# Optimization experiments

Hardware: AMD Instinct MI355X
Metric: run time of the kernel (lower is better)

The kernel has to match this reference:

```python
import jax, jax.numpy as jnp
import numpy as np

H, W = 256, 256
N_PIXELS = H * W
MAX_DIST = float(np.sqrt(H ** 2 + W ** 2))
RESIZED = jnp.array([H, W], dtype=jnp.float32)

# all_img_locations: cartesian product of rows x cols, shape [N_PIXELS, 2] as (row, col)
_rr, _cc = jnp.meshgrid(jnp.arange(H), jnp.arange(W), indexing='ij')
LOCS = jnp.stack([_rr, _cc], axis=-1).reshape(-1, 2).astype(jnp.float32)


def setup_inputs() -> dict:
    key = jax.random.key(0)
    k1, k2, k3 = jax.random.split(key, 3)
    B, M = 8, 128
    # probability map in open interval (0,1) so log(p) and log(1-p) are finite
    prob_map = jnp.clip(jax.random.uniform(k1, (B, H, W), dtype=jnp.float32), 1e-4, 1.0 - 1e-4)
    # gt heatmap: mostly <1 with a sprinkling of exact 1.0 'center' pixels (so pos_count > 0)
    u = jax.random.uniform(k2, (B, H, W), dtype=jnp.float32)
    gt_map = jnp.where(u > 0.999, jnp.float32(1.0), u * 0.999)
    # ground-truth points (row, col) in [0, H) x [0, W)
    gt = jax.random.uniform(k3, (B, M, 2), dtype=jnp.float32) * RESIZED
    # original image sizes (height, width)
    orig_sizes = jnp.ones((B, 2), dtype=jnp.float32) * 1024.0
    return {"prob_map": prob_map, "gt_map": gt_map, "gt": gt, "orig_sizes": orig_sizes}


def _center_focal_loss(pred, g, alpha=2, beta=4):
    pos = (g == 1.0).astype(pred.dtype)
    neg = (g < 1.0).astype(pred.dtype)
    pos_term = (1.0 - pred) ** alpha * jnp.log(pred) * pos
    neg_term = (1.0 - g) ** beta * pred ** alpha * jnp.log1p(-pred) * neg
    return -((pos_term + neg_term).sum() / pos.sum())


def _whd_terms(pm_b, gt_b, orig_size_b):
    norm = orig_size_b / RESIZED                      # [2]
    nx = LOCS * norm                                  # [N, 2]
    ny = gt_b * norm                                  # [M, 2]
    diff = nx[:, None, :] - ny[None, :, :]            # [N, M, 2]
    d = jnp.sqrt(jnp.sum(diff * diff, axis=-1))       # [N, M]
    p = pm_b.reshape(-1)                              # [N]
    n_est = p.sum()
    term1 = jnp.sum(p * d.min(axis=1)) / (n_est + 1e-6)
    weighted = (1.0 - p)[:, None] * MAX_DIST + p[:, None] * d
    term2 = weighted.min(axis=0).mean()               # generalized mean reduces to min over pixels
    return term1, term2


def reference(prob_map, gt_map, gt, orig_sizes):
    terms_1, terms_2 = jax.vmap(_whd_terms)(prob_map, gt, orig_sizes)
    # original loop overwrites terms_3 each iteration -> only last batch element's focal loss survives
    terms_3 = _center_focal_loss(prob_map[-1], gt_map[-1])
    return terms_1.mean() + terms_2.mean() + terms_3
```

## Files before the change

kernel.cpp:

```cpp
#include <hip/hip_runtime.h>
#include <math.h>


#define HH 256
#define WW 256
#define NPIX (HH*WW)
#define MM 128
#define BB 8
#define MAXDIST 362.03867196751236f
#define PBLK 128
#define NBLK (BB*PBLK)
#define TPB 256
#define NW 4
#define MW 32
#define PIXB 512
#define POISON 0xAAAAAAAAu
#define LASTTOK (POISON + (unsigned)(NBLK - 1))

__device__ __forceinline__ float fast_sqrt(float x) {
  float r;
  asm("v_sqrt_f32 %0, %1" : "=v"(r) : "v"(x));
  return r;
}

__device__ __forceinline__ float wave_sum(float v) {
#pragma unroll
  for (int off = 32; off > 0; off >>= 1) v += __shfl_xor(v, off, 64);
  return v;
}

__global__ __launch_bounds__(TPB, 4) void whd_fused(
    const float* __restrict__ prob, const float* __restrict__ gtmap,
    const float* __restrict__ gt, const float* __restrict__ osz,
    unsigned* __restrict__ colmin,
    float* __restrict__ partials,
    unsigned* __restrict__ counter,
    float* __restrict__ out) {
  const int b    = blockIdx.x >> 7;
  const int blk  = blockIdx.x & (PBLK - 1);
  const int tid  = threadIdx.x;
  const int lane = tid & 63;
  const int w    = tid >> 6;

  __shared__ float2 sgt[MM];
  __shared__ float  sp[PIXB];
  __shared__ float  mdw[NW * PIXB];
  __shared__ float  scm[MM];
  __shared__ float  wred[NW][4];
  __shared__ int    lastFlag;
  __shared__ float  sT[NW];
  __shared__ float  sA[BB], sC[BB], sF[BB], sG[BB];

  const float ny = osz[b * 2 + 0] * (1.0f / HH);
  const float nx = osz[b * 2 + 1] * (1.0f / WW);

  if (tid < MM) {
    float gy = gt[(b * MM + tid) * 2 + 0] * ny;
    float gx = gt[(b * MM + tid) * 2 + 1] * nx;
    sgt[tid] = make_float2(gy, gx);
  }

  const int pixBase = blk * PIXB + tid * 2;
  const float2 pv = *(const float2*)(prob + b * NPIX + pixBase);
  const float p0 = pv.x, p1 = pv.y;
  sp[tid * 2] = p0;
  sp[tid * 2 + 1] = p1;
  const float spsum = p0 + p1;
  float fs = 0.0f, fc = 0.0f;
  if (b == BB - 1) {
    const float2 gv = *(const float2*)(gtmap + b * NPIX + pixBase);
    {
      float g = gv.x, pi = p0;
      if (g == 1.0f) { float om = 1.0f - pi; fs += om * om * logf(pi); fc += 1.0f; }
      else { float t = 1.0f - g, t2 = t * t; fs += t2 * t2 * pi * pi * log1pf(-pi); }
    }
    {
      float g = gv.y, pi = p1;
      if (g == 1.0f) { float om = 1.0f - pi; fs += om * om * logf(pi); fc += 1.0f; }
      else { float t = 1.0f - g, t2 = t * t; fs += t2 * t2 * pi * pi * log1pf(-pi); }
    }
  }
  __syncthreads();

  const float pyf0 = (float)(2 * blk) * ny;
  const float pyf1 = (float)(2 * blk + 1) * ny;
  float gxr[MW], dy2[MW], cm[MW];
#pragma unroll
  for (int j = 0; j < MW; j++) {
    float2 g2 = sgt[w * MW + j];
    gxr[j] = g2.y;
    cm[j]  = 3.0e38f;
    float dy = pyf0 - g2.x;
    dy2[j] = dy * dy;
  }

#pragma unroll 1
  for (int g = 0; g < 8; g++) {
    if (g == 4) {
#pragma unroll
      for (int j = 0; j < MW; j++) {
        float dy = pyf1 - sgt[w * MW + j].x;
        dy2[j] = dy * dy;
      }
    }
    const float pp = sp[g * 64 + lane];
    const float bi = (1.0f - pp) * MAXDIST;
    const float xi = (float)(((g & 3) << 6) + lane) * nx;
    float md0 = 3.0e38f, md1 = 3.0e38f;
#pragma unroll
    for (int j = 0; j < MW; j += 2) {
      float dx0 = xi - gxr[j];
      float d0  = fast_sqrt(fmaf(dx0, dx0, dy2[j]));
      md0   = fminf(md0, d0);
      cm[j] = fminf(cm[j], fmaf(pp, d0, bi));
      float dx1 = xi - gxr[j + 1];
      float d1  = fast_sqrt(fmaf(dx1, dx1, dy2[j + 1]));
      md1       = fminf(md1, d1);
      cm[j + 1] = fminf(cm[j + 1], fmaf(pp, d1, bi));
    }
    mdw[w * PIXB + g * 64 + lane] = fminf(md0, md1);
  }

  {
    const bool h5 = (lane & 32) != 0;
#pragma unroll
    for (int k = 0; k < 16; k++) {
      float keep = h5 ? cm[k + 16] : cm[k];
      float send = h5 ? cm[k] : cm[k + 16];
      cm[k] = fminf(keep, __shfl_xor(send, 32, 64));
    }
    const bool h4 = (lane & 16) != 0;
#pragma unroll
    for (int k = 0; k < 8; k++) {
      float keep = h4 ? cm[k + 8] : cm[k];
      float send = h4 ? cm[k] : cm[k + 8];
      cm[k] = fminf(keep, __shfl_xor(send, 16, 64));
    }
    const bool h3 = (lane & 8) != 0;
#pragma unroll
    for (int k = 0; k < 4; k++) {
      float keep = h3 ? cm[k + 4] : cm[k];
      float send = h3 ? cm[k] : cm[k + 4];
      cm[k] = fminf(keep, __shfl_xor(send, 8, 64));
    }
    const bool h2 = (lane & 4) != 0;
#pragma unroll
    for (int k = 0; k < 2; k++) {
      float keep = h2 ? cm[k + 2] : cm[k];
      float send = h2 ? cm[k] : cm[k + 2];
      cm[k] = fminf(keep, __shfl_xor(send, 4, 64));
    }
    const bool h1 = (lane & 2) != 0;
    {
      float keep = h1 ? cm[1] : cm[0];
      float send = h1 ? cm[0] : cm[1];
      cm[0] = fminf(keep, __shfl_xor(send, 2, 64));
    }
    float v = fminf(cm[0], __shfl_xor(cm[0], 1, 64));
    if ((lane & 1) == 0) scm[w * MW + ((lane >> 1) & 31)] = v;
  }
  __syncthreads();

  const int px0 = 2 * tid, px1 = 2 * tid + 1;
  float mdf0 = fminf(fminf(mdw[0 * PIXB + px0], mdw[1 * PIXB + px0]),
                     fminf(mdw[2 * PIXB + px0], mdw[3 * PIXB + px0]));
  float mdf1 = fminf(fminf(mdw[0 * PIXB + px1], mdw[1 * PIXB + px1]),
                     fminf(mdw[2 * PIXB + px1], mdw[3 * PIXB + px1]));
  float spd = 0.0f;
  spd = fmaf(p0, mdf0, spd);
  spd = fmaf(p1, mdf1, spd);

  if (tid < MM) atomicMin(&colmin[b * MM + tid], __float_as_uint(scm[tid]));

  spd = wave_sum(spd);
  float spw = wave_sum(spsum);
  fs = wave_sum(fs);
  fc = wave_sum(fc);
  if (lane == 0) {
    wred[w][0] = spd; wred[w][1] = spw; wred[w][2] = fs; wred[w][3] = fc;
  }
  __syncthreads();

  if (tid == 0) {
    float a = 0, c2 = 0, e = 0, f = 0;
#pragma unroll
    for (int wv = 0; wv < NW; wv++) {
      a += wred[wv][0]; c2 += wred[wv][1]; e += wred[wv][2]; f += wred[wv][3];
    }
    float* pt = partials + blockIdx.x * 4;
    pt[0] = a; pt[1] = c2; pt[2] = e; pt[3] = f;
    __threadfence();
    unsigned old = atomicAdd(counter, 1u);
    lastFlag = (old == LASTTOK) ? 1 : 0;
  }
  __syncthreads();
  if (lastFlag == 0) return;

  __threadfence();

  float s = 0.0f;
  for (int i = tid; i < BB * MM; i += TPB)
    s += __uint_as_float(atomicAdd(&colmin[i], 0u));
  s = wave_sum(s);
  if (lane == 0) sT[w] = s;

  const int gb = tid >> 5;
  const int i  = tid & 31;
  float a = 0, c = 0, e = 0, f = 0;
  for (int k = i; k < PBLK; k += 32) {
    float* pt = partials + (gb * PBLK + k) * 4;
    a += atomicAdd(pt + 0, 0.0f);
    c += atomicAdd(pt + 1, 0.0f);
    e += atomicAdd(pt + 2, 0.0f);
    f += atomicAdd(pt + 3, 0.0f);
  }
#pragma unroll
  for (int off = 16; off > 0; off >>= 1) {
    a += __shfl_xor(a, off, 64); c += __shfl_xor(c, off, 64);
    e += __shfl_xor(e, off, 64); f += __shfl_xor(f, off, 64);
  }
  if (i == 0) { sA[gb] = a; sC[gb] = c; sF[gb] = e; sG[gb] = f; }
  __syncthreads();

  if (tid == 0) {
    float t2 = (sT[0] + sT[1] + sT[2] + sT[3]) * (1.0f / (BB * MM));
    float t1 = 0.0f;
    for (int b2 = 0; b2 < BB; b2++) t1 += sA[b2] / (sC[b2] + 1e-6f);
    t1 *= (1.0f / BB);
    float fsum = 0.0f, fcnt = 0.0f;
    for (int b2 = 0; b2 < BB; b2++) { fsum += sF[b2]; fcnt += sG[b2]; }
    out[0] = t1 + t2 - fsum / fcnt;
  }
}

extern "C" void kernel_launch(void* const* d_in, const int* in_sizes, int n_in,
                              void* d_out, int out_size, void* d_ws, size_t ws_size,
                              hipStream_t stream) {
  const float* prob  = (const float*)d_in[0];
  const float* gtmap = (const float*)d_in[1];
  const float* gt    = (const float*)d_in[2];
  const float* osz   = (const float*)d_in[3];
  float* out = (float*)d_out;

  unsigned* colmin  = (unsigned*)d_ws;
  float* partials   = (float*)((char*)d_ws + 4096);
  unsigned* counter = (unsigned*)((char*)d_ws + 4096 + NBLK * 16);

  whd_fused<<<NBLK, TPB, 0, stream>>>(prob, gtmap, gt, osz, colmin, partials,
                                      counter, out);
}
```

Baseline: 86.24 us.

## Double threads per block, split GT points over 8 waves, defer row-min sqrt

Raises the block to 512 threads with 8 waves, each handling 16 ground-truth points instead of 32, so each thread loads one pixel and holds fewer per-point registers. The per-pixel minimum over GT points is now taken on squared distances, and a single sqrt is applied after the cross-wave reduction, though the per-pair sqrt is still needed for the column term. The cross-lane column-min butterfly is shortened to match, and the final reduction is guarded for the extra thread groups. This trades more waves per block and an 8-way shared-memory min for better occupancy and less register pressure.

Result: slower. 90.23 us (+4.6%).

```diff
diff --git a/kernel.cpp b/kernel.cpp
--- a/kernel.cpp
+++ b/kernel.cpp
@@ -10,9 +10,9 @@
 #define MAXDIST 362.03867196751236f
 #define PBLK 128
 #define NBLK (BB*PBLK)
-#define TPB 256
-#define NW 4
-#define MW 32
+#define TPB 512
+#define NW 8
+#define MW 16
 #define PIXB 512
 #define POISON 0xAAAAAAAAu
 #define LASTTOK (POISON + (unsigned)(NBLK - 1))
@@ -60,25 +60,14 @@
     sgt[tid] = make_float2(gy, gx);
   }
 
-  const int pixBase = blk * PIXB + tid * 2;
-  const float2 pv = *(const float2*)(prob + b * NPIX + pixBase);
-  const float p0 = pv.x, p1 = pv.y;
-  sp[tid * 2] = p0;
-  sp[tid * 2 + 1] = p1;
-  const float spsum = p0 + p1;
+  const int px = blk * PIXB + tid;
+  const float p0 = prob[b * NPIX + px];
+  sp[tid] = p0;
   float fs = 0.0f, fc = 0.0f;
   if (b == BB - 1) {
-    const float2 gv = *(const float2*)(gtmap + b * NPIX + pixBase);
-    {
-      float g = gv.x, pi = p0;
-      if (g == 1.0f) { float om = 1.0f - pi; fs += om * om * logf(pi); fc += 1.0f; }
-      else { float t = 1.0f - g, t2 = t * t; fs += t2 * t2 * pi * pi * log1pf(-pi); }
-    }
-    {
-      float g = gv.y, pi = p1;
-      if (g == 1.0f) { float om = 1.0f - pi; fs += om * om * logf(pi); fc += 1.0f; }
-      else { float t = 1.0f - g, t2 = t * t; fs += t2 * t2 * pi * pi * log1pf(-pi); }
-    }
+    float g = gtmap[b * NPIX + px];
+    if (g == 1.0f) { float om = 1.0f - p0; fs = om * om * logf(p0); fc = 1.0f; }
+    else { float t = 1.0f - g, t2 = t * t; fs = t2 * t2 * p0 * p0 * log1pf(-p0); }
   }
   __syncthreads();
 
@@ -110,12 +99,14 @@
 #pragma unroll
     for (int j = 0; j < MW; j += 2) {
       float dx0 = xi - gxr[j];
-      float d0  = fast_sqrt(fmaf(dx0, dx0, dy2[j]));
-      md0   = fminf(md0, d0);
+      float s0  = fmaf(dx0, dx0, dy2[j]);
+      md0 = fminf(md0, s0);
+      float d0  = fast_sqrt(s0);
       cm[j] = fminf(cm[j], fmaf(pp, d0, bi));
       float dx1 = xi - gxr[j + 1];
-      float d1  = fast_sqrt(fmaf(dx1, dx1, dy2[j + 1]));
-      md1       = fminf(md1, d1);
+      float s1  = fmaf(dx1, dx1, dy2[j + 1]);
+      md1 = fminf(md1, s1);
+      float d1  = fast_sqrt(s1);
       cm[j + 1] = fminf(cm[j + 1], fmaf(pp, d1, bi));
     }
     mdw[w * PIXB + g * 64 + lane] = fminf(md0, md1);
@@ -124,56 +115,46 @@
   {
     const bool h5 = (lane & 32) != 0;
 #pragma unroll
-    for (int k = 0; k < 16; k++) {
-      float keep = h5 ? cm[k + 16] : cm[k];
-      float send = h5 ? cm[k] : cm[k + 16];
+    for (int k = 0; k < 8; k++) {
+      float keep = h5 ? cm[k + 8] : cm[k];
+      float send = h5 ? cm[k] : cm[k + 8];
       cm[k] = fminf(keep, __shfl_xor(send, 32, 64));
     }
     const bool h4 = (lane & 16) != 0;
 #pragma unroll
-    for (int k = 0; k < 8; k++) {
-      float keep = h4 ? cm[k + 8] : cm[k];
-      float send = h4 ? cm[k] : cm[k + 8];
+    for (int k = 0; k < 4; k++) {
+      float keep = h4 ? cm[k + 4] : cm[k];
+      float send = h4 ? cm[k] : cm[k + 4];
       cm[k] = fminf(keep, __shfl_xor(send, 16, 64));
     }
     const bool h3 = (lane & 8) != 0;
 #pragma unroll
-    for (int k = 0; k < 4; k++) {
-      float keep = h3 ? cm[k + 4] : cm[k];
-      float send = h3 ? cm[k] : cm[k + 4];
+    for (int k = 0; k < 2; k++) {
+      float keep = h3 ? cm[k + 2] : cm[k];
+      float send = h3 ? cm[k] : cm[k + 2];
       cm[k] = fminf(keep, __shfl_xor(send, 8, 64));
     }
     const bool h2 = (lane & 4) != 0;
-#pragma unroll
-    for (int k = 0; k < 2; k++) {
-      float keep = h2 ? cm[k + 2] : cm[k];
-      float send = h2 ? cm[k] : cm[k + 2];
-      cm[k] = fminf(keep, __shfl_xor(send, 4, 64));
-    }
-    const bool h1 = (lane & 2) != 0;
     {
-      float keep = h1 ? cm[1] : cm[0];
-      float send = h1 ? cm[0] : cm[1];
-      cm[0] = fminf(keep, __shfl_xor(send, 2, 64));
+      float keep = h2 ? cm[1] : cm[0];
+      float send = h2 ? cm[0] : cm[1];
+      cm[0] = fminf(keep, __shfl_xor(send, 4, 64));
     }
     float v = fminf(cm[0], __shfl_xor(cm[0], 1, 64));
-    if ((lane & 1) == 0) scm[w * MW + ((lane >> 1) & 31)] = v;
-  }
-  __syncthreads();
-
-  const int px0 = 2 * tid, px1 = 2 * tid + 1;
-  float mdf0 = fminf(fminf(mdw[0 * PIXB + px0], mdw[1 * PIXB + px0]),
-                     fminf(mdw[2 * PIXB + px0], mdw[3 * PIXB + px0]));
-  float mdf1 = fminf(fminf(mdw[0 * PIXB + px1], mdw[1 * PIXB + px1]),
-                     fminf(mdw[2 * PIXB + px1], mdw[3 * PIXB + px1]));
-  float spd = 0.0f;
-  spd = fmaf(p0, mdf0, spd);
-  spd = fmaf(p1, mdf1, spd);
+    v = fminf(v, __shfl_xor(v, 2, 64));
+    if ((lane & 3) == 0) scm[w * MW + (lane >> 2)] = v;
+  }
+  __syncthreads();
+
+  float m2 = mdw[tid];
+#pragma unroll
+  for (int wv = 1; wv < NW; wv++) m2 = fminf(m2, mdw[wv * PIXB + tid]);
+  float spd = p0 * fast_sqrt(m2);
 
   if (tid < MM) atomicMin(&colmin[b * MM + tid], __float_as_uint(scm[tid]));
 
   spd = wave_sum(spd);
-  float spw = wave_sum(spsum);
+  float spw = wave_sum(p0);
   fs = wave_sum(fs);
   fc = wave_sum(fc);
   if (lane == 0) {
@@ -199,31 +180,36 @@
   __threadfence();
 
   float s = 0.0f;
-  for (int i = tid; i < BB * MM; i += TPB)
-    s += __uint_as_float(atomicAdd(&colmin[i], 0u));
+  for (int i2 = tid; i2 < BB * MM; i2 += TPB)
+    s += __uint_as_float(atomicAdd(&colmin[i2], 0u));
   s = wave_sum(s);
   if (lane == 0) sT[w] = s;
 
   const int gb = tid >> 5;
-  const int i  = tid & 31;
+  const int ii = tid & 31;
   float a = 0, c = 0, e = 0, f = 0;
-  for (int k = i; k < PBLK; k += 32) {
-    float* pt = partials + (gb * PBLK + k) * 4;
-    a += atomicAdd(pt + 0, 0.0f);
-    c += atomicAdd(pt + 1, 0.0f);
-    e += atomicAdd(pt + 2, 0.0f);
-    f += atomicAdd(pt + 3, 0.0f);
+  if (gb < BB) {
+    for (int k = ii; k < PBLK; k += 32) {
+      float* pt = partials + (gb * PBLK + k) * 4;
+      a += atomicAdd(pt + 0, 0.0f);
+      c += atomicAdd(pt + 1, 0.0f);
+      e += atomicAdd(pt + 2, 0.0f);
+      f += atomicAdd(pt + 3, 0.0f);
+    }
   }
 #pragma unroll
   for (int off = 16; off > 0; off >>= 1) {
     a += __shfl_xor(a, off, 64); c += __shfl_xor(c, off, 64);
     e += __shfl_xor(e, off, 64); f += __shfl_xor(f, off, 64);
   }
-  if (i == 0) { sA[gb] = a; sC[gb] = c; sF[gb] = e; sG[gb] = f; }
+  if (gb < BB && ii == 0) { sA[gb] = a; sC[gb] = c; sF[gb] = e; sG[gb] = f; }
   __syncthreads();
 
   if (tid == 0) {
-    float t2 = (sT[0] + sT[1] + sT[2] + sT[3]) * (1.0f / (BB * MM));
+    float t2 = 0.0f;
+#pragma unroll
+    for (int wv = 0; wv < NW; wv++) t2 += sT[wv];
+    t2 *= (1.0f / (BB * MM));
     float t1 = 0.0f;
     for (int b2 = 0; b2 < BB; b2++) t1 += sA[b2] / (sC[b2] + 1e-6f);
     t1 *= (1.0f / BB);
```
